# Performance work log

Hardware: AMD Instinct MI355X
Metric: run time of the kernel (lower is better)

Reference implementation:

```python
import jax, jax.numpy as jnp
import numpy as np

H = 128        # hidden_size
V = 100000     # item vocab
B = 1024       # sessions
NODES = 32     # unique nodes per session (sections)
ITEMS = 16     # itemsets per session (sequence_len)
P = 8          # PADDED_LENGTH
N = B * NODES  # total nodes
T = B * ITEMS  # total itemsets


def setup_inputs() -> dict:
    key = jax.random.key(0)
    ks = jax.random.split(key, 10)
    s = 1.0 / np.sqrt(H)
    node_embedding = jax.random.normal(ks[0], (N, H), jnp.float32)
    emb_weight = jax.random.normal(ks[1], (V, H), jnp.float32) * s
    W1_w = jax.random.normal(ks[2], (H, H), jnp.float32) * s
    W1_b = jnp.zeros((H,), jnp.float32)
    W2_w = jax.random.normal(ks[3], (H, H), jnp.float32) * s
    W2_b = jnp.zeros((H,), jnp.float32)
    q_w = jax.random.normal(ks[4], (1, H), jnp.float32) * s
    q_b = jnp.zeros((1,), jnp.float32)
    W3_w = jax.random.normal(ks[5], (H, 2 * H), jnp.float32) * s
    W3_b = jnp.zeros((H,), jnp.float32)
    batch = jnp.repeat(jnp.arange(B, dtype=jnp.int32), NODES)  # sorted segment ids
    # local node indices per itemset; value == NODES means padding (zero row)
    sequence = jax.random.randint(ks[6], (T, P), 0, NODES + 1, jnp.int32)
    sequence = sequence.at[:, 0].set(jnp.minimum(sequence[:, 0], NODES - 1))  # >=1 valid entry
    itemset_len = jnp.sum(sequence < NODES, axis=1).astype(jnp.int32)
    sequence_len = jnp.full((B,), ITEMS, jnp.int32)
    cue = jax.random.randint(ks[7], (B,), 0, V, jnp.int32)
    return dict(node_embedding=node_embedding, emb_weight=emb_weight,
                W1_w=W1_w, W1_b=W1_b, W2_w=W2_w, W2_b=W2_b,
                q_w=q_w, q_b=q_b, W3_w=W3_w, W3_b=W3_b,
                batch=batch, sequence=sequence, itemset_len=itemset_len,
                sequence_len=sequence_len, cue=cue)


def reference(node_embedding, emb_weight, W1_w, W1_b, W2_w, W2_b,
              q_w, q_b, W3_w, W3_b, batch, sequence, itemset_len,
              sequence_len, cue):
    nB = sequence_len.shape[0]
    nN = node_embedding.shape[0]
    nT = sequence.shape[0]
    # per-session node counts (torch.bincount) and exclusive offsets (torch.split)
    sections = jax.ops.segment_sum(jnp.ones_like(batch), batch, num_segments=nB)
    node_off = jnp.cumsum(sections) - sections                      # [B]
    # session id of each itemset (torch.split(sequence, sequence_len))
    seq_cum = jnp.cumsum(sequence_len)                              # [B]
    itemset_seg = jnp.searchsorted(seq_cum, jnp.arange(nT), side='right')  # [T]
    # gather: local index == sections[s] hits the appended zero row -> mask to 0
    sec_t = sections[itemset_seg][:, None]                          # [T,1]
    valid = sequence < sec_t                                        # [T,P]
    gidx = jnp.clip(node_off[itemset_seg][:, None] + sequence, 0, nN - 1)
    gathered = jnp.where(valid[..., None], node_embedding[gidx], 0.0)  # [T,P,H]
    itemset_emb = gathered.sum(axis=1) / itemset_len[:, None].astype(node_embedding.dtype)  # [T,H]
    # last itemset of each session = v_n
    v_n = itemset_emb[seq_cum - 1]                                  # [B,H]
    v_n_rep = v_n[itemset_seg]                                      # [T,H]
    gate = jax.nn.sigmoid(v_n_rep @ W1_w.T + W1_b + itemset_emb @ W2_w.T + W2_b)
    alpha = gate @ q_w.T + q_b                                      # [T,1]
    s_g = jax.ops.segment_sum(alpha * itemset_emb, itemset_seg, num_segments=nB)  # [B,H]
    s_h = jnp.concatenate([v_n, s_g], axis=1) @ W3_w.T + W3_b       # [B,H]
    y_hat = jnp.sum(s_h * emb_weight[cue], axis=1)                  # [B]
    all_scores = s_h @ emb_weight.T                                 # [B,V]
    return (y_hat, all_scores)
```

## Files before the change

kernel.cpp:

```cpp
#include <hip/hip_runtime.h>
#include <hip/hip_bf16.h>

#define H 128
#define VOCAB 100000
#define B_SESS 1024
#define NODES 32
#define ITEMS 16
#define PADLEN 8
#define NCHUNK 32

typedef short short8 __attribute__((ext_vector_type(8)));
typedef float f32x16 __attribute__((ext_vector_type(16)));
typedef float f32x4 __attribute__((ext_vector_type(4)));

static __device__ __forceinline__ short f2bf(float x) {
    unsigned u = __builtin_bit_cast(unsigned, x);
    u += 0x7fffu + ((u >> 16) & 1u);
    return (short)(u >> 16);
}

__global__ __launch_bounds__(256) void k_transpose(
    const float* __restrict__ W1, const float* __restrict__ W2,
    const float* __restrict__ W3,
    float* __restrict__ W1t, float* __restrict__ W2t, float* __restrict__ W3t)
{
    const int idx = blockIdx.x * 256 + threadIdx.x;
    const int k = idx >> 7, j = idx & 127;
    W1t[idx] = W1[j * H + k];
    W2t[idx] = W2[j * H + k];
    W3t[k * H + j]       = W3[j * 2 * H + k];
    W3t[(k + H) * H + j] = W3[j * 2 * H + k + H];
}

__global__ __launch_bounds__(H) void k_session(
    const float* __restrict__ node_emb,
    const int* __restrict__ sequence,
    const int* __restrict__ itemset_len,
    const float* __restrict__ W1t, const float* __restrict__ W1_b,
    const float* __restrict__ W2t, const float* __restrict__ W2_b,
    const float* __restrict__ q_w,  const float* __restrict__ q_b,
    const float* __restrict__ W3t, const float* __restrict__ W3_b,
    const float* __restrict__ emb_weight, const int* __restrict__ cue,
    float* __restrict__ y_hat, short* __restrict__ packA)
{
    __shared__ float it[ITEMS][H];
    __shared__ float contrib[ITEMS][H];
    __shared__ float red[ITEMS][8];
    __shared__ float alphas[ITEMS];
    __shared__ float sg[H];
    __shared__ float wred[2];

    const int b = blockIdx.x;
    const int j = threadIdx.x;
    const int nbase = b * NODES;

#pragma unroll
    for (int t = 0; t < ITEMS; ++t) {
        const int tg = b * ITEMS + t;
        float acc = 0.f;
#pragma unroll
        for (int p = 0; p < PADLEN; ++p) {
            int s = sequence[tg * PADLEN + p];
            if (s < NODES) acc += node_emb[(nbase + s) * H + j];
        }
        it[t][j] = acc / (float)itemset_len[tg];
    }
    __syncthreads();

    float pre = W1_b[j] + W2_b[j];
#pragma unroll 4
    for (int k = 0; k < H; k += 4) {
        float4 v = *(const float4*)&it[ITEMS - 1][k];
        pre += W1t[(k + 0) * H + j] * v.x + W1t[(k + 1) * H + j] * v.y
             + W1t[(k + 2) * H + j] * v.z + W1t[(k + 3) * H + j] * v.w;
    }

    float h2[ITEMS];
#pragma unroll
    for (int t = 0; t < ITEMS; ++t) h2[t] = 0.f;
    for (int k = 0; k < H; k += 4) {
        float w0 = W2t[(k + 0) * H + j];
        float w1 = W2t[(k + 1) * H + j];
        float w2 = W2t[(k + 2) * H + j];
        float w3 = W2t[(k + 3) * H + j];
#pragma unroll
        for (int t = 0; t < ITEMS; ++t) {
            float4 v = *(const float4*)&it[t][k];
            h2[t] += w0 * v.x + w1 * v.y + w2 * v.z + w3 * v.w;
        }
    }

    const float qwj = q_w[j];
#pragma unroll
    for (int t = 0; t < ITEMS; ++t) {
        float g = 1.f / (1.f + __expf(-(pre + h2[t])));
        contrib[t][j] = qwj * g;
    }
    __syncthreads();

    {
        int t = j >> 3, part = j & 7;
        float s = 0.f;
#pragma unroll
        for (int u = 0; u < 16; ++u) s += contrib[t][part * 16 + u];
        red[t][part] = s;
    }
    __syncthreads();
    if (j < ITEMS) {
        float s = q_b[0];
#pragma unroll
        for (int u = 0; u < 8; ++u) s += red[j][u];
        alphas[j] = s;
    }
    __syncthreads();

    float sgj = 0.f;
#pragma unroll
    for (int t = 0; t < ITEMS; ++t) sgj += alphas[t] * it[t][j];
    sg[j] = sgj;
    __syncthreads();

    float sh = W3_b[j];
#pragma unroll 4
    for (int k = 0; k < H; k += 4) {
        float4 v = *(const float4*)&it[ITEMS - 1][k];
        sh += W3t[(k + 0) * H + j] * v.x + W3t[(k + 1) * H + j] * v.y
            + W3t[(k + 2) * H + j] * v.z + W3t[(k + 3) * H + j] * v.w;
    }
#pragma unroll 4
    for (int k = 0; k < H; k += 4) {
        float4 v = *(const float4*)&sg[k];
        sh += W3t[(H + k + 0) * H + j] * v.x + W3t[(H + k + 1) * H + j] * v.y
            + W3t[(H + k + 2) * H + j] * v.z + W3t[(H + k + 3) * H + j] * v.w;
    }

    {
        const int c = b >> 5, cl = b & 31;
        const int s = j >> 4, hi = (j >> 3) & 1, i = j & 7;
        packA[c * 4096 + s * 512 + hi * 256 + cl * 8 + i] = f2bf(sh);
    }

    float prod = sh * emb_weight[(long)cue[b] * H + j];
#pragma unroll
    for (int off = 32; off > 0; off >>= 1) prod += __shfl_down(prod, off);
    if ((j & 63) == 0) wred[j >> 6] = prod;
    __syncthreads();
    if (j == 0) y_hat[b] = wred[0] + wred[1];
}

__global__ __launch_bounds__(256, 4) void k_scores(
    const float* __restrict__ emb_weight,
    const short* __restrict__ packA,
    float* __restrict__ scores)
{
    const int bid = blockIdx.x;

    const int wave = threadIdx.x >> 6;
    const int lane = threadIdx.x & 63;
    const int hi = lane >> 5;
    const int cl = lane & 31;
    const int col = bid * 128 + wave * 32 + cl;
    const bool valid = col < VOCAB;

    short8 bfrag[8];
    if (valid) {
        const float* row = emb_weight + (long)col * H;
#pragma unroll
        for (int s = 0; s < 8; ++s) {
            const f32x4* p = (const f32x4*)(row + s * 16 + hi * 8);
            f32x4 x = p[0];
            f32x4 y = p[1];
            short8 f;
            f[0] = f2bf(x[0]); f[1] = f2bf(x[1]); f[2] = f2bf(x[2]); f[3] = f2bf(x[3]);
            f[4] = f2bf(y[0]); f[5] = f2bf(y[1]); f[6] = f2bf(y[2]); f[7] = f2bf(y[3]);
            bfrag[s] = f;
        }
    } else {
#pragma unroll
        for (int s = 0; s < 8; ++s) {
            short8 z;
#pragma unroll
            for (int i = 0; i < 8; ++i) z[i] = 0;
            bfrag[s] = z;
        }
    }

    for (int c = 0; c < NCHUNK; ++c) {
        const short* ap = packA + c * 4096 + hi * 256 + cl * 8;
        short8 a[8];
#pragma unroll
        for (int s = 0; s < 8; ++s) a[s] = *(const short8*)(ap + s * 512);
        f32x16 acc;
#pragma unroll
        for (int r2 = 0; r2 < 16; ++r2) acc[r2] = 0.f;
#pragma unroll
        for (int s = 0; s < 8; ++s)
            acc = __builtin_amdgcn_mfma_f32_32x32x16_bf16(a[s], bfrag[s], acc, 0, 0, 0);
        if (valid) {
            const int M0 = c * 32;
#pragma unroll
            for (int r2 = 0; r2 < 16; ++r2) {
                int rowm = (r2 & 3) + 8 * (r2 >> 2) + 4 * hi;
                __builtin_nontemporal_store(acc[r2],
                    &scores[(long)(M0 + rowm) * VOCAB + col]);
            }
        }
    }
}

extern "C" void kernel_launch(void* const* d_in, const int* in_sizes, int n_in,
                              void* d_out, int out_size, void* d_ws, size_t ws_size,
                              hipStream_t stream) {
    const float* node_emb   = (const float*)d_in[0];
    const float* emb_w      = (const float*)d_in[1];
    const float* W1_w       = (const float*)d_in[2];
    const float* W1_b       = (const float*)d_in[3];
    const float* W2_w       = (const float*)d_in[4];
    const float* W2_b       = (const float*)d_in[5];
    const float* q_w        = (const float*)d_in[6];
    const float* q_b        = (const float*)d_in[7];
    const float* W3_w       = (const float*)d_in[8];
    const float* W3_b       = (const float*)d_in[9];
    const int* sequence     = (const int*)d_in[11];
    const int* itemset_len  = (const int*)d_in[12];
    const int* cue          = (const int*)d_in[14];

    float* out    = (float*)d_out;
    float* y_hat  = out;
    float* scores = out + B_SESS;

    short* packA = (short*)d_ws;
    float* W1t   = (float*)((char*)d_ws + (256 << 10));
    float* W2t   = W1t + H * H;
    float* W3t   = W2t + H * H;

    k_transpose<<<64, 256, 0, stream>>>(W1_w, W2_w, W3_w, W1t, W2t, W3t);
    k_session<<<B_SESS, H, 0, stream>>>(node_emb, sequence, itemset_len,
                                        W1t, W1_b, W2t, W2_b,
                                        q_w, q_b, W3t, W3_b, emb_w, cue,
                                        y_hat, packA);
    const int nblk = (VOCAB + 127) / 128;
    k_scores<<<nblk, 256, 0, stream>>>(emb_w, packA, scores);
}
```

Before: 142.5 us.

## Process one session per wavefront using register broadcasts instead of shared memory

The session kernel now gives each 64-lane wavefront a whole session, with each lane owning two hidden columns. Itemset embeddings live in registers and are broadcast with readlane, and the alpha and y_hat reductions use xor shuffles. This drops all shared memory and block-wide barriers. In exchange it raises register pressure and serializes readlane broadcasts, while the large score GEMM kernel stays unchanged.

Result: slower. 166.8 us (+17.0%).

```diff
diff --git a/kernel.cpp b/kernel.cpp
--- a/kernel.cpp
+++ b/kernel.cpp
@@ -17,6 +17,11 @@
     unsigned u = __builtin_bit_cast(unsigned, x);
     u += 0x7fffu + ((u >> 16) & 1u);
     return (short)(u >> 16);
+}
+
+static __device__ __forceinline__ float rdlane(float x, int k) {
+    return __builtin_bit_cast(float,
+        __builtin_amdgcn_readlane(__builtin_bit_cast(int, x), k));
 }
 
 __global__ __launch_bounds__(256) void k_transpose(
@@ -32,7 +37,7 @@
     W3t[(k + H) * H + j] = W3[j * 2 * H + k + H];
 }
 
-__global__ __launch_bounds__(H) void k_session(
+__global__ __launch_bounds__(128) void k_session(
     const float* __restrict__ node_emb,
     const int* __restrict__ sequence,
     const int* __restrict__ itemset_len,
@@ -43,109 +48,131 @@
     const float* __restrict__ emb_weight, const int* __restrict__ cue,
     float* __restrict__ y_hat, short* __restrict__ packA)
 {
-    __shared__ float it[ITEMS][H];
-    __shared__ float contrib[ITEMS][H];
-    __shared__ float red[ITEMS][8];
-    __shared__ float alphas[ITEMS];
-    __shared__ float sg[H];
-    __shared__ float wred[2];
-
-    const int b = blockIdx.x;
-    const int j = threadIdx.x;
+    const int b = blockIdx.x * 2 + (threadIdx.x >> 6);
+    const int l = threadIdx.x & 63;
+    const int ja = l, jb = l + 64;
     const int nbase = b * NODES;
 
+    float it_a[ITEMS], it_b[ITEMS];
 #pragma unroll
     for (int t = 0; t < ITEMS; ++t) {
         const int tg = b * ITEMS + t;
-        float acc = 0.f;
+        float aa = 0.f, ab = 0.f;
 #pragma unroll
         for (int p = 0; p < PADLEN; ++p) {
             int s = sequence[tg * PADLEN + p];
-            if (s < NODES) acc += node_emb[(nbase + s) * H + j];
-        }
-        it[t][j] = acc / (float)itemset_len[tg];
-    }
-    __syncthreads();
-
-    float pre = W1_b[j] + W2_b[j];
-#pragma unroll 4
-    for (int k = 0; k < H; k += 4) {
-        float4 v = *(const float4*)&it[ITEMS - 1][k];
-        pre += W1t[(k + 0) * H + j] * v.x + W1t[(k + 1) * H + j] * v.y
-             + W1t[(k + 2) * H + j] * v.z + W1t[(k + 3) * H + j] * v.w;
-    }
-
-    float h2[ITEMS];
-#pragma unroll
-    for (int t = 0; t < ITEMS; ++t) h2[t] = 0.f;
-    for (int k = 0; k < H; k += 4) {
-        float w0 = W2t[(k + 0) * H + j];
-        float w1 = W2t[(k + 1) * H + j];
-        float w2 = W2t[(k + 2) * H + j];
-        float w3 = W2t[(k + 3) * H + j];
+            if (s < NODES) {
+                const float* row = node_emb + (size_t)(nbase + s) * H;
+                aa += row[ja];
+                ab += row[jb];
+            }
+        }
+        float len = (float)itemset_len[tg];
+        it_a[t] = aa / len;
+        it_b[t] = ab / len;
+    }
+
+    float pre_a = W1_b[ja] + W2_b[ja];
+    float pre_b = W1_b[jb] + W2_b[jb];
+#pragma unroll 8
+    for (int k = 0; k < 64; ++k) {
+        float vn = rdlane(it_a[ITEMS - 1], k);
+        pre_a = fmaf(W1t[k * H + ja], vn, pre_a);
+        pre_b = fmaf(W1t[k * H + jb], vn, pre_b);
+    }
+#pragma unroll 8
+    for (int k = 64; k < H; ++k) {
+        float vn = rdlane(it_b[ITEMS - 1], k - 64);
+        pre_a = fmaf(W1t[k * H + ja], vn, pre_a);
+        pre_b = fmaf(W1t[k * H + jb], vn, pre_b);
+    }
+
+    float h2a[ITEMS], h2b[ITEMS];
+#pragma unroll
+    for (int t = 0; t < ITEMS; ++t) { h2a[t] = 0.f; h2b[t] = 0.f; }
+#pragma unroll 2
+    for (int k = 0; k < 64; ++k) {
+        float wa = W2t[k * H + ja];
+        float wb = W2t[k * H + jb];
 #pragma unroll
         for (int t = 0; t < ITEMS; ++t) {
-            float4 v = *(const float4*)&it[t][k];
-            h2[t] += w0 * v.x + w1 * v.y + w2 * v.z + w3 * v.w;
-        }
-    }
-
-    const float qwj = q_w[j];
+            float s = rdlane(it_a[t], k);
+            h2a[t] = fmaf(wa, s, h2a[t]);
+            h2b[t] = fmaf(wb, s, h2b[t]);
+        }
+    }
+#pragma unroll 2
+    for (int k = 64; k < H; ++k) {
+        float wa = W2t[k * H + ja];
+        float wb = W2t[k * H + jb];
+#pragma unroll
+        for (int t = 0; t < ITEMS; ++t) {
+            float s = rdlane(it_b[t], k - 64);
+            h2a[t] = fmaf(wa, s, h2a[t]);
+            h2b[t] = fmaf(wb, s, h2b[t]);
+        }
+    }
+
+    const float qa = q_w[ja], qb2 = q_w[jb];
+    const float qbias = q_b[0];
+    float alpha[ITEMS];
 #pragma unroll
     for (int t = 0; t < ITEMS; ++t) {
-        float g = 1.f / (1.f + __expf(-(pre + h2[t])));
-        contrib[t][j] = qwj * g;
-    }
-    __syncthreads();
-
-    {
-        int t = j >> 3, part = j & 7;
-        float s = 0.f;
-#pragma unroll
-        for (int u = 0; u < 16; ++u) s += contrib[t][part * 16 + u];
-        red[t][part] = s;
-    }
-    __syncthreads();
-    if (j < ITEMS) {
-        float s = q_b[0];
-#pragma unroll
-        for (int u = 0; u < 8; ++u) s += red[j][u];
-        alphas[j] = s;
-    }
-    __syncthreads();
-
-    float sgj = 0.f;
-#pragma unroll
-    for (int t = 0; t < ITEMS; ++t) sgj += alphas[t] * it[t][j];
-    sg[j] = sgj;
-    __syncthreads();
-
-    float sh = W3_b[j];
-#pragma unroll 4
-    for (int k = 0; k < H; k += 4) {
-        float4 v = *(const float4*)&it[ITEMS - 1][k];
-        sh += W3t[(k + 0) * H + j] * v.x + W3t[(k + 1) * H + j] * v.y
-            + W3t[(k + 2) * H + j] * v.z + W3t[(k + 3) * H + j] * v.w;
-    }
-#pragma unroll 4
-    for (int k = 0; k < H; k += 4) {
-        float4 v = *(const float4*)&sg[k];
-        sh += W3t[(H + k + 0) * H + j] * v.x + W3t[(H + k + 1) * H + j] * v.y
-            + W3t[(H + k + 2) * H + j] * v.z + W3t[(H + k + 3) * H + j] * v.w;
+        float ga = 1.f / (1.f + __expf(-(pre_a + h2a[t])));
+        float gb = 1.f / (1.f + __expf(-(pre_b + h2b[t])));
+        float c = qa * ga + qb2 * gb;
+#pragma unroll
+        for (int off = 32; off > 0; off >>= 1) c += __shfl_xor(c, off);
+        alpha[t] = qbias + c;
+    }
+
+    float sga = 0.f, sgb = 0.f;
+#pragma unroll
+    for (int t = 0; t < ITEMS; ++t) {
+        sga = fmaf(alpha[t], it_a[t], sga);
+        sgb = fmaf(alpha[t], it_b[t], sgb);
+    }
+
+    float sha = W3_b[ja], shb = W3_b[jb];
+#pragma unroll 8
+    for (int k = 0; k < 64; ++k) {
+        float vn = rdlane(it_a[ITEMS - 1], k);
+        sha = fmaf(W3t[k * H + ja], vn, sha);
+        shb = fmaf(W3t[k * H + jb], vn, shb);
+    }
+#pragma unroll 8
+    for (int k = 64; k < H; ++k) {
+        float vn = rdlane(it_b[ITEMS - 1], k - 64);
+        sha = fmaf(W3t[k * H + ja], vn, sha);
+        shb = fmaf(W3t[k * H + jb], vn, shb);
+    }
+#pragma unroll 8
+    for (int k = 0; k < 64; ++k) {
+        float sg = rdlane(sga, k);
+        sha = fmaf(W3t[(H + k) * H + ja], sg, sha);
+        shb = fmaf(W3t[(H + k) * H + jb], sg, shb);
+    }
+#pragma unroll 8
+    for (int k = 64; k < H; ++k) {
+        float sg = rdlane(sgb, k - 64);
+        sha = fmaf(W3t[(H + k) * H + ja], sg, sha);
+        shb = fmaf(W3t[(H + k) * H + jb], sg, shb);
     }
 
     {
         const int c = b >> 5, cl = b & 31;
-        const int s = j >> 4, hi = (j >> 3) & 1, i = j & 7;
-        packA[c * 4096 + s * 512 + hi * 256 + cl * 8 + i] = f2bf(sh);
-    }
-
-    float prod = sh * emb_weight[(long)cue[b] * H + j];
-#pragma unroll
-    for (int off = 32; off > 0; off >>= 1) prod += __shfl_down(prod, off);
-    if ((j & 63) == 0) wred[j >> 6] = prod;
-    __syncthreads();
-    if (j == 0) y_hat[b] = wred[0] + wred[1];
+        const int base = c * 4096 + cl * 8;
+        packA[base + (ja >> 4) * 512 + ((ja >> 3) & 1) * 256 + (ja & 7)] = f2bf(sha);
+        packA[base + (jb >> 4) * 512 + ((jb >> 3) & 1) * 256 + (jb & 7)] = f2bf(shb);
+    }
+
+    {
+        const float* er = emb_weight + (long)cue[b] * H;
+        float prod = sha * er[ja] + shb * er[jb];
+#pragma unroll
+        for (int off = 32; off > 0; off >>= 1) prod += __shfl_xor(prod, off);
+        if (l == 0) y_hat[b] = prod;
+    }
 }
 
 __global__ __launch_bounds__(256, 4) void k_scores(
@@ -235,10 +262,10 @@
     float* W3t   = W2t + H * H;
 
     k_transpose<<<64, 256, 0, stream>>>(W1_w, W2_w, W3_w, W1t, W2t, W3t);
-    k_session<<<B_SESS, H, 0, stream>>>(node_emb, sequence, itemset_len,
-                                        W1t, W1_b, W2t, W2_b,
-                                        q_w, q_b, W3t, W3_b, emb_w, cue,
-                                        y_hat, packA);
+    k_session<<<B_SESS / 2, 128, 0, stream>>>(node_emb, sequence, itemset_len,
+                                              W1t, W1_b, W2t, W2_b,
+                                              q_w, q_b, W3t, W3_b, emb_w, cue,
+                                              y_hat, packA);
     const int nblk = (VOCAB + 127) / 128;
     k_scores<<<nblk, 256, 0, stream>>>(emb_w, packA, scores);
 }
```

## Compute W2 gate projection with bf16 MFMA and fuse alpha reduction via shuffles

Applied to the files above, without the earlier changes.

The per-session 16x128x128 W2 projection moves from scalar FP32 FMA loops to bf16 16x16x32 MFMA instructions. W2 is read in its original layout, so its transpose is dropped. The gate sigmoid and q_w dot product are reduced with warp shuffles rather than a two-stage LDS reduction, which removes a shared buffer and a barrier. This lowers the precision of the gate computation to bf16 inputs. The scores kernel, which likely dominates total time, is unchanged.

After: 135.9 us (median of 2 runs). 4.7% less time.

```diff
diff --git a/kernel.cpp b/kernel.cpp
--- a/kernel.cpp
+++ b/kernel.cpp
@@ -19,15 +19,20 @@
     return (short)(u >> 16);
 }
 
+static __device__ __forceinline__ short8 pack8(f32x4 x, f32x4 y) {
+    short8 f;
+    f[0] = f2bf(x[0]); f[1] = f2bf(x[1]); f[2] = f2bf(x[2]); f[3] = f2bf(x[3]);
+    f[4] = f2bf(y[0]); f[5] = f2bf(y[1]); f[6] = f2bf(y[2]); f[7] = f2bf(y[3]);
+    return f;
+}
+
 __global__ __launch_bounds__(256) void k_transpose(
-    const float* __restrict__ W1, const float* __restrict__ W2,
-    const float* __restrict__ W3,
-    float* __restrict__ W1t, float* __restrict__ W2t, float* __restrict__ W3t)
+    const float* __restrict__ W1, const float* __restrict__ W3,
+    float* __restrict__ W1t, float* __restrict__ W3t)
 {
     const int idx = blockIdx.x * 256 + threadIdx.x;
     const int k = idx >> 7, j = idx & 127;
     W1t[idx] = W1[j * H + k];
-    W2t[idx] = W2[j * H + k];
     W3t[k * H + j]       = W3[j * 2 * H + k];
     W3t[(k + H) * H + j] = W3[j * 2 * H + k + H];
 }
@@ -37,17 +42,17 @@
     const int* __restrict__ sequence,
     const int* __restrict__ itemset_len,
     const float* __restrict__ W1t, const float* __restrict__ W1_b,
-    const float* __restrict__ W2t, const float* __restrict__ W2_b,
+    const float* __restrict__ W2_w, const float* __restrict__ W2_b,
     const float* __restrict__ q_w,  const float* __restrict__ q_b,
     const float* __restrict__ W3t, const float* __restrict__ W3_b,
     const float* __restrict__ emb_weight, const int* __restrict__ cue,
     float* __restrict__ y_hat, short* __restrict__ packA)
 {
     __shared__ float it[ITEMS][H];
-    __shared__ float contrib[ITEMS][H];
-    __shared__ float red[ITEMS][8];
+    __shared__ float pre_lds[H];
+    __shared__ float sg[H];
     __shared__ float alphas[ITEMS];
-    __shared__ float sg[H];
+    __shared__ float apart[2][ITEMS];
     __shared__ float wred[2];
 
     const int b = blockIdx.x;
@@ -67,57 +72,71 @@
     }
     __syncthreads();
 
-    float pre = W1_b[j] + W2_b[j];
+    {
+        float pre = W1_b[j] + W2_b[j];
 #pragma unroll 4
-    for (int k = 0; k < H; k += 4) {
-        float4 v = *(const float4*)&it[ITEMS - 1][k];
-        pre += W1t[(k + 0) * H + j] * v.x + W1t[(k + 1) * H + j] * v.y
-             + W1t[(k + 2) * H + j] * v.z + W1t[(k + 3) * H + j] * v.w;
-    }
-
-    float h2[ITEMS];
-#pragma unroll
-    for (int t = 0; t < ITEMS; ++t) h2[t] = 0.f;
-    for (int k = 0; k < H; k += 4) {
-        float w0 = W2t[(k + 0) * H + j];
-        float w1 = W2t[(k + 1) * H + j];
-        float w2 = W2t[(k + 2) * H + j];
-        float w3 = W2t[(k + 3) * H + j];
-#pragma unroll
-        for (int t = 0; t < ITEMS; ++t) {
-            float4 v = *(const float4*)&it[t][k];
-            h2[t] += w0 * v.x + w1 * v.y + w2 * v.z + w3 * v.w;
-        }
-    }
-
-    const float qwj = q_w[j];
-#pragma unroll
-    for (int t = 0; t < ITEMS; ++t) {
-        float g = 1.f / (1.f + __expf(-(pre + h2[t])));
-        contrib[t][j] = qwj * g;
-    }
-    __syncthreads();
-
-    {
-        int t = j >> 3, part = j & 7;
-        float s = 0.f;
-#pragma unroll
-        for (int u = 0; u < 16; ++u) s += contrib[t][part * 16 + u];
-        red[t][part] = s;
-    }
-    __syncthreads();
-    if (j < ITEMS) {
-        float s = q_b[0];
-#pragma unroll
-        for (int u = 0; u < 8; ++u) s += red[j][u];
-        alphas[j] = s;
-    }
-    __syncthreads();
-
-    float sgj = 0.f;
-#pragma unroll
-    for (int t = 0; t < ITEMS; ++t) sgj += alphas[t] * it[t][j];
-    sg[j] = sgj;
+        for (int k = 0; k < H; k += 4) {
+            float4 v = *(const float4*)&it[ITEMS - 1][k];
+            pre += W1t[(k + 0) * H + j] * v.x + W1t[(k + 1) * H + j] * v.y
+                 + W1t[(k + 2) * H + j] * v.z + W1t[(k + 3) * H + j] * v.w;
+        }
+        pre_lds[j] = pre;
+    }
+    __syncthreads();
+
+    {
+        const int w = threadIdx.x >> 6;
+        const int l = threadIdx.x & 63;
+        const int tA = l & 15, kg = l >> 4;
+
+        short8 afr[4];
+#pragma unroll
+        for (int s = 0; s < 4; ++s) {
+            const f32x4* p = (const f32x4*)&it[tA][s * 32 + kg * 8];
+            afr[s] = pack8(p[0], p[1]);
+        }
+
+        f32x4 hacc[4];
+        float qwc[4];
+#pragma unroll
+        for (int nt = 0; nt < 4; ++nt) {
+            const int jcol = (w * 4 + nt) * 16 + (l & 15);
+            qwc[nt] = q_w[jcol];
+#pragma unroll
+            for (int r = 0; r < 4; ++r) hacc[nt][r] = 0.f;
+#pragma unroll
+            for (int s = 0; s < 4; ++s) {
+                const float* wr = W2_w + jcol * H + s * 32 + kg * 8;
+                short8 bfr = pack8(*(const f32x4*)wr, *(const f32x4*)(wr + 4));
+                hacc[nt] = __builtin_amdgcn_mfma_f32_16x16x32_bf16(
+                    afr[s], bfr, hacc[nt], 0, 0, 0);
+            }
+        }
+#pragma unroll
+        for (int r = 0; r < 4; ++r) {
+            float s = 0.f;
+#pragma unroll
+            for (int nt = 0; nt < 4; ++nt) {
+                const int jcol = (w * 4 + nt) * 16 + (l & 15);
+                float g = 1.f / (1.f + __expf(-(pre_lds[jcol] + hacc[nt][r])));
+                s = fmaf(qwc[nt], g, s);
+            }
+            s += __shfl_xor(s, 1); s += __shfl_xor(s, 2);
+            s += __shfl_xor(s, 4); s += __shfl_xor(s, 8);
+            if ((l & 15) == 0) apart[w][kg * 4 + r] = s;
+        }
+    }
+    __syncthreads();
+    if (threadIdx.x < ITEMS)
+        alphas[threadIdx.x] = q_b[0] + apart[0][threadIdx.x] + apart[1][threadIdx.x];
+    __syncthreads();
+
+    {
+        float sgj = 0.f;
+#pragma unroll
+        for (int t = 0; t < ITEMS; ++t) sgj = fmaf(alphas[t], it[t][j], sgj);
+        sg[j] = sgj;
+    }
     __syncthreads();
 
     float sh = W3_b[j];
@@ -168,12 +187,7 @@
 #pragma unroll
         for (int s = 0; s < 8; ++s) {
             const f32x4* p = (const f32x4*)(row + s * 16 + hi * 8);
-            f32x4 x = p[0];
-            f32x4 y = p[1];
-            short8 f;
-            f[0] = f2bf(x[0]); f[1] = f2bf(x[1]); f[2] = f2bf(x[2]); f[3] = f2bf(x[3]);
-            f[4] = f2bf(y[0]); f[5] = f2bf(y[1]); f[6] = f2bf(y[2]); f[7] = f2bf(y[3]);
-            bfrag[s] = f;
+            bfrag[s] = pack8(p[0], p[1]);
         }
     } else {
 #pragma unroll
@@ -231,12 +245,11 @@
 
     short* packA = (short*)d_ws;
     float* W1t   = (float*)((char*)d_ws + (256 << 10));
-    float* W2t   = W1t + H * H;
-    float* W3t   = W2t + H * H;
-
-    k_transpose<<<64, 256, 0, stream>>>(W1_w, W2_w, W3_w, W1t, W2t, W3t);
+    float* W3t   = W1t + H * H;
+
+    k_transpose<<<64, 256, 0, stream>>>(W1_w, W3_w, W1t, W3t);
     k_session<<<B_SESS, H, 0, stream>>>(node_emb, sequence, itemset_len,
-                                        W1t, W1_b, W2t, W2_b,
+                                        W1t, W1_b, W2_w, W2_b,
                                         q_w, q_b, W3t, W3_b, emb_w, cue,
                                         y_hat, packA);
     const int nblk = (VOCAB + 127) / 128;
```
